# Kernel tuning notes

Measured on AMD Instinct MI355X. Metric: run time of the kernel, lower is better.

The kernel has to match this reference:

```python
import jax, jax.numpy as jnp
import numpy as np

ALPHA = 0.1        # dt / tau = 1 / 10
SIGMA_REC = 0.03
SIGMA_INP = 0.03


def setup_inputs() -> dict:
    key = jax.random.key(0)
    ks = jax.random.split(key, 7)
    n, N, num_inputs, num_outputs, T, B = 128, 1024, 6, 2, 512, 256
    u = jax.random.normal(ks[0], (num_inputs, T, B), dtype=jnp.float32)
    rec_noise = jax.random.normal(ks[1], (B, T, n), dtype=jnp.float32)
    inp_noise = jax.random.normal(ks[2], (B, T, num_inputs), dtype=jnp.float32)
    W_inp = jax.random.normal(ks[3], (n, num_inputs), dtype=jnp.float32) / np.float32(np.sqrt(num_inputs))
    # spectral-ish scaling keeps the leaky RNN stable over 512 steps
    W_rec = jax.random.normal(ks[4], (n, n), dtype=jnp.float32) * np.float32(0.9 / np.sqrt(n))
    W_out = jax.random.normal(ks[5], (num_outputs, n), dtype=jnp.float32) / np.float32(np.sqrt(n))
    # q is orthonormalized via SVD in the torch module (make_orthonormal)
    q0 = np.asarray(jax.random.uniform(ks[6], (n, N)), dtype=np.float32)
    U, _, Vh = np.linalg.svd(q0, full_matrices=False)
    q = jnp.asarray((U @ Vh).astype(np.float32))
    return dict(u=u, rec_noise=rec_noise, inp_noise=inp_noise,
                W_inp=W_inp, W_rec=W_rec, W_out=W_out, q=q)


def reference(u, rec_noise, inp_noise, W_inp, W_rec, W_out, q):
    # u: (num_inputs, T, B); noise tensors already batch-major (B, T, .)
    B = u.shape[-1]
    n = W_rec.shape[0]
    rn = jnp.sqrt(2.0 / ALPHA * SIGMA_REC ** 2) * rec_noise      # (B, T, n)
    inoise = jnp.sqrt(2.0 / ALPHA * SIGMA_INP ** 2) * inp_noise  # (B, T, num_inputs)
    ub = jnp.swapaxes(u, 0, -1)                                  # (B, T, num_inputs)
    x0 = jnp.zeros((B, n), dtype=u.dtype)                        # initial state self.x = 0

    def step(x, ins):
        u_t, in_t, rn_t = ins
        x_new = (1.0 - ALPHA) * x + ALPHA * (
            jax.nn.relu(x @ W_rec.T + (u_t + in_t) @ W_inp.T) + rn_t)
        return x_new, x_new

    # T-1 update steps using inputs at t = 0 .. T-2 (matches the torch loop)
    xs_in = (jnp.swapaxes(ub, 0, 1)[:-1],
             jnp.swapaxes(inoise, 0, 1)[:-1],
             jnp.swapaxes(rn, 0, 1)[:-1])
    _, xs = jax.lax.scan(step, x0, xs_in)                        # (T-1, B, n)
    states = jnp.concatenate([x0[:, None, :], jnp.swapaxes(xs, 0, 1)], axis=1)  # (B, T, n)

    outputs = jnp.swapaxes(states @ W_out.T, 0, -1)              # (num_outputs, T, B)
    states_embedded = jnp.swapaxes(states @ q, 0, -1)            # (N, T, B)
    return states_embedded, outputs
```

## Files before the change

kernel.cpp:

```cpp
#include <hip/hip_runtime.h>
#include <hip/hip_bf16.h>

#define T_STEPS 512
#define BATCH   256
#define NN      128
#define NEMB    1024
#define M_ROWS  (T_STEPS * BATCH)
#define NOISE_K 0.13416407864998738f
#define NB      16
#define CH      4
#define NSTEP   (T_STEPS - 1)
#define NCH     ((NSTEP + CH - 1) / CH)

typedef short s16x8 __attribute__((ext_vector_type(8)));
typedef float f32x4 __attribute__((ext_vector_type(4)));
typedef int   s32x2 __attribute__((ext_vector_type(2)));
typedef int   s32x4 __attribute__((ext_vector_type(4)));

union FragU { s32x4 i4; s16x8 s8; };

__device__ __forceinline__ unsigned short f2bf(float f) {
  union { float f; unsigned u; } v; v.f = f;
  unsigned r = v.u + 0x7fffu + ((v.u >> 16) & 1u);
  return (unsigned short)(r >> 16);
}
__device__ __forceinline__ float bf2f(unsigned short s) {
  union { unsigned u; float f; } v; v.u = ((unsigned)s) << 16;
  return v.f;
}
__device__ __forceinline__ unsigned pkbf(float lo, float hi) {
  __hip_bfloat162 h = __float22bfloat162_rn(float2{lo, hi});
  union { __hip_bfloat162 h; unsigned u; } c; c.h = h; return c.u;
}

__device__ __forceinline__ void light_barrier() {
  asm volatile("s_waitcnt lgkmcnt(0)" ::: "memory");
  __builtin_amdgcn_s_barrier();
  asm volatile("" ::: "memory");
}

__global__ __launch_bounds__(256, 1) void rnn_mfma_kernel(
    const float* __restrict__ u,
    const float* __restrict__ rec_noise,
    const float* __restrict__ inp_noise,
    const float* __restrict__ W_inp,
    const float* __restrict__ W_rec,
    unsigned short* __restrict__ states)
{
  const int b0  = blockIdx.x * NB;
  const int tid = threadIdx.x;
  const int wv  = tid >> 6;
  const int l   = tid & 63;
  const int lr  = l & 15;
  const int lg  = l >> 4;

  __shared__ char           xld[2][32 * 136];
  __shared__ float          rns[2][NB * CH * 128];
  __shared__ unsigned short uinl[NB * CH * 8];

  const int mf0 = wv * 2;
  s16x8 wA[2][5];
  #pragma unroll
  for (int mi = 0; mi < 2; ++mi) {
    const int mf = mf0 + mi;
    const float* wrow = W_rec + (size_t)(mf * 16 + lr) * NN;
    #pragma unroll
    for (int kc = 0; kc < 4; ++kc) {
      f32x4 v0 = *(const f32x4*)(wrow + kc * 32 + lg * 8);
      f32x4 v1 = *(const f32x4*)(wrow + kc * 32 + lg * 8 + 4);
      FragU f;
      f.i4 = s32x4{(int)pkbf(v0.x, v0.y), (int)pkbf(v0.z, v0.w),
                   (int)pkbf(v1.x, v1.y), (int)pkbf(v1.z, v1.w)};
      wA[mi][kc] = f.s8;
    }
    float wi[6] = {0.f, 0.f, 0.f, 0.f, 0.f, 0.f};
    if (lg == 0) {
      #pragma unroll
      for (int j = 0; j < 6; ++j) wi[j] = W_inp[(mf * 16 + lr) * 6 + j];
    }
    FragU f;
    f.i4 = s32x4{(int)pkbf(wi[0], wi[1]), (int)pkbf(wi[2], wi[3]),
                 (int)pkbf(wi[4], wi[5]), 0};
    wA[mi][4] = f.s8;
  }

  for (int i = tid; i < 1088; i += 256) ((int*)&xld[0][0])[i] = 0;
  *(s32x4*)((char*)states + (size_t)b0 * 256 + tid * 16) = s32x4{0, 0, 0, 0};

  int loff[8];
  #pragma unroll
  for (int s = 0; s < 8; ++s)
    loff[s] = (l >> 5) * 512 + (((l & 31) * 16) ^ (s << 4));

  #pragma unroll
  for (int bb = 0; bb < 4; ++bb) {
    const int b = wv * 4 + bb;
    const char* gb = (const char*)rec_noise +
                     ((size_t)(b0 + b) * T_STEPS + 0) * 512 + loff[b & 7];
    float* db = &rns[0][b * 512];
    __builtin_amdgcn_global_load_lds(
        (const __attribute__((address_space(1))) void*)gb,
        (__attribute__((address_space(3))) void*)db, 16, 0, 0);
    __builtin_amdgcn_global_load_lds(
        (const __attribute__((address_space(1))) void*)(gb + 1024),
        (__attribute__((address_space(3))) void*)(db + 256), 16, 0, 0);
  }
  float uu[6], ii[6];
  if (wv == 0) {
    #pragma unroll
    for (int j = 0; j < 6; ++j) {
      uu[j] = u[(size_t)j * (T_STEPS * BATCH) + (size_t)lg * BATCH + b0 + lr];
      ii[j] = inp_noise[((size_t)(b0 + lr) * T_STEPS + lg) * 6 + j];
    }
  }
  asm volatile("s_waitcnt vmcnt(0)" ::: "memory");
  if (wv == 0) {
    *(s32x2*)&uinl[(lr * 4 + lg) * 8] =
        s32x2{(int)pkbf(uu[0] + NOISE_K * ii[0], uu[1] + NOISE_K * ii[1]),
              (int)pkbf(uu[2] + NOISE_K * ii[2], uu[3] + NOISE_K * ii[3])};
    *(s32x2*)&uinl[(lr * 4 + lg) * 8 + 4] =
        s32x2{(int)pkbf(uu[4] + NOISE_K * ii[4], uu[5] + NOISE_K * ii[5]), 0};
  }
  __syncthreads();

  float xo[2][4];
  #pragma unroll
  for (int mi = 0; mi < 2; ++mi)
    #pragma unroll
    for (int r = 0; r < 4; ++r) xo[mi][r] = 0.f;

  for (int c = 0; c < NCH; ++c) {
    const int  cb   = c & 1;
    const bool more = (c + 1 < NCH);

    if (more) {
      const int t0n = (c + 1) * CH;
      #pragma unroll
      for (int bb = 0; bb < 4; ++bb) {
        const int b = wv * 4 + bb;
        const char* gb = (const char*)rec_noise +
                         ((size_t)(b0 + b) * T_STEPS + t0n) * 512 + loff[b & 7];
        float* db = &rns[cb ^ 1][b * 512];
        __builtin_amdgcn_global_load_lds(
            (const __attribute__((address_space(1))) void*)gb,
            (__attribute__((address_space(3))) void*)db, 16, 0, 0);
        __builtin_amdgcn_global_load_lds(
            (const __attribute__((address_space(1))) void*)(gb + 1024),
            (__attribute__((address_space(3))) void*)(db + 256), 16, 0, 0);
      }
      if (wv == 0) {
        const int tb = t0n + lg;
        #pragma unroll
        for (int j = 0; j < 6; ++j) {
          uu[j] = u[(size_t)j * (T_STEPS * BATCH) + (size_t)tb * BATCH + b0 + lr];
          ii[j] = inp_noise[((size_t)(b0 + lr) * T_STEPS + tb) * 6 + j];
        }
      }
    }

    #pragma unroll
    for (int ts = 0; ts < CH; ++ts) {
      const int t = c * CH + ts;
      if (t >= NSTEP) break;
      const int cur = t & 1, nxt = cur ^ 1;

      s16x8 xb[4];
      #pragma unroll
      for (int kc = 0; kc < 4; ++kc) {
        const char* p = xld[cur] + (kc * 8 + lg * 2) * 136 + lr * 8;
        s32x2 r1 = *(const s32x2*)p;
        s32x2 r2 = *(const s32x2*)(p + 136);
        FragU f; f.i4 = s32x4{r1.x, r1.y, r2.x, r2.y};
        xb[kc] = f.s8;
      }
      FragU uf; uf.i4 = *(const s32x4*)&uinl[(lr * 4 + ts) * 8];
      const s16x8 ub = (lg == 0) ? uf.s8 : s16x8{0, 0, 0, 0, 0, 0, 0, 0};

      unsigned short* srow =
          states + ((size_t)(t + 1) * BATCH + b0 + lr) * NN + lg * 4;

      #pragma unroll
      for (int mi = 0; mi < 2; ++mi) {
        const int mf = mf0 + mi;
        f32x4 a = f32x4{0.f, 0.f, 0.f, 0.f};
        a = __builtin_amdgcn_mfma_f32_16x16x32_bf16(wA[mi][0], xb[0], a, 0, 0, 0);
        a = __builtin_amdgcn_mfma_f32_16x16x32_bf16(wA[mi][1], xb[1], a, 0, 0, 0);
        a = __builtin_amdgcn_mfma_f32_16x16x32_bf16(wA[mi][2], xb[2], a, 0, 0, 0);
        a = __builtin_amdgcn_mfma_f32_16x16x32_bf16(wA[mi][3], xb[3], a, 0, 0, 0);
        a = __builtin_amdgcn_mfma_f32_16x16x32_bf16(wA[mi][4], ub,    a, 0, 0, 0);
        const f32x4 rn4 = *(const f32x4*)&rns[cb][lr * 512 + ts * 128 +
                               ((mf * 16 + lg * 4) ^ ((lr & 7) << 2))];
        float xn[4];
        #pragma unroll
        for (int r = 0; r < 4; ++r) {
          const float rl = fmaxf(a[r], 0.f);
          xn[r] = 0.9f * xo[mi][r] + 0.1f * (rl + NOISE_K * rn4[r]);
          xo[mi][r] = xn[r];
        }
        const s32x2 pw{(int)pkbf(xn[0], xn[1]), (int)pkbf(xn[2], xn[3])};
        *(s32x2*)(xld[nxt] + (mf * 4 + lg) * 136 + lr * 8) = pw;
        *(s32x2*)(srow + mf * 16) = pw;
      }
      light_barrier();
    }

    if (more) {
      asm volatile("s_waitcnt vmcnt(8)" ::: "memory");
      if (wv == 0) {
        *(s32x2*)&uinl[(lr * 4 + lg) * 8] =
            s32x2{(int)pkbf(uu[0] + NOISE_K * ii[0], uu[1] + NOISE_K * ii[1]),
                  (int)pkbf(uu[2] + NOISE_K * ii[2], uu[3] + NOISE_K * ii[3])};
        *(s32x2*)&uinl[(lr * 4 + lg) * 8 + 4] =
            s32x2{(int)pkbf(uu[4] + NOISE_K * ii[4], uu[5] + NOISE_K * ii[5]), 0};
      }
      light_barrier();
    }
  }
}

__global__ __launch_bounds__(256) void emb_kernel(
    const unsigned short* __restrict__ states,
    const float* __restrict__ q,
    const float* __restrict__ W_out,
    float* __restrict__ out)
{
  const int jt  = blockIdx.x;
  const int mt  = blockIdx.y;
  const int tid = threadIdx.x;
  const int w   = tid >> 6;
  const int l   = tid & 63;
  const int lg  = l >> 4;
  const int lr  = l & 15;

  __shared__ unsigned short qt[64 * 128];
  __shared__ float wos[2 * NN];

  {
    const int j  = tid & 63;
    const int k0 = tid >> 6;
    #pragma unroll
    for (int kk = k0; kk < 128; kk += 4) {
      float v = q[kk * NEMB + jt * 64 + j];
      int k8 = kk >> 3, e = kk & 7;
      qt[j * 128 + ((k8 ^ (j & 7)) << 3) + e] = f2bf(v);
    }
  }
  if (jt == 0) wos[tid] = W_out[tid];

  s16x8 afrag[2][4];
  #pragma unroll
  for (int mf = 0; mf < 2; ++mf) {
    const int m = mt * 128 + w * 32 + mf * 16 + lr;
    const unsigned short* arow = states + m * NN;
    #pragma unroll
    for (int kc = 0; kc < 4; ++kc)
      afrag[mf][kc] = *(const s16x8*)(arow + kc * 32 + lg * 8);
  }
  __syncthreads();

  f32x4 acc[2][4] = {};
  #pragma unroll
  for (int kc = 0; kc < 4; ++kc) {
    s16x8 bfrag[4];
    #pragma unroll
    for (int jf = 0; jf < 4; ++jf) {
      const int jl = jf * 16 + lr;
      bfrag[jf] = *(const s16x8*)(qt + jl * 128 + ((((kc << 2) + lg) ^ (jl & 7)) << 3));
    }
    #pragma unroll
    for (int mf = 0; mf < 2; ++mf)
      #pragma unroll
      for (int jf = 0; jf < 4; ++jf)
        acc[mf][jf] = __builtin_amdgcn_mfma_f32_16x16x32_bf16(
            afrag[mf][kc], bfrag[jf], acc[mf][jf], 0, 0, 0);
  }

  if (jt == 0) {
    #pragma unroll
    for (int mf = 0; mf < 2; ++mf) {
      float s0 = 0.f, s1 = 0.f;
      #pragma unroll
      for (int kc = 0; kc < 4; ++kc) {
        const int kb = kc * 32 + lg * 8;
        const s16x8 af = afrag[mf][kc];
        #pragma unroll
        for (int e = 0; e < 8; ++e) {
          const float x = bf2f((unsigned short)af[e]);
          s0 = fmaf(x, wos[kb + e], s0);
          s1 = fmaf(x, wos[NN + kb + e], s1);
        }
      }
      s0 += __shfl_xor(s0, 16); s0 += __shfl_xor(s0, 32);
      s1 += __shfl_xor(s1, 16); s1 += __shfl_xor(s1, 32);
      if (lg == 0) {
        const long m = (long)mt * 128 + w * 32 + mf * 16 + lr;
        out[(long)1024 * M_ROWS + m] = s0;
        out[(long)1025 * M_ROWS + m] = s1;
      }
    }
  }

  #pragma unroll
  for (int mf = 0; mf < 2; ++mf) {
    const int m = mt * 128 + w * 32 + mf * 16 + lg * 4;
    #pragma unroll
    for (int jf = 0; jf < 4; ++jf) {
      const long j = jt * 64 + jf * 16 + lr;
      *(f32x4*)&out[j * M_ROWS + m] = acc[mf][jf];
    }
  }
}

extern "C" void kernel_launch(void* const* d_in, const int* in_sizes, int n_in,
                              void* d_out, int out_size, void* d_ws, size_t ws_size,
                              hipStream_t stream) {
  const float* u         = (const float*)d_in[0];
  const float* rec_noise = (const float*)d_in[1];
  const float* inp_noise = (const float*)d_in[2];
  const float* W_inp     = (const float*)d_in[3];
  const float* W_rec     = (const float*)d_in[4];
  const float* W_out     = (const float*)d_in[5];
  const float* q         = (const float*)d_in[6];
  float* out = (float*)d_out;
  unsigned short* states = (unsigned short*)d_ws;

  rnn_mfma_kernel<<<dim3(BATCH / NB), dim3(256), 0, stream>>>(
      u, rec_noise, inp_noise, W_inp, W_rec, states);

  dim3 g2(NEMB / 64, M_ROWS / 128);
  emb_kernel<<<g2, dim3(256), 0, stream>>>(states, q, W_out, out);
}
```

Measured before the change: 501.9 us.

## Fuse recurrence and embedding GEMM into one producer-consumer persistent kernel

Result: slower. 518.3 us (+3.3%).

```diff
diff --git a/kernel.cpp b/kernel.cpp
--- a/kernel.cpp
+++ b/kernel.cpp
@@ -11,6 +11,8 @@
 #define CH      4
 #define NSTEP   (T_STEPS - 1)
 #define NCH     ((NSTEP + CH - 1) / CH)
+#define NPROD   16
+#define NCONS   240
 
 typedef short s16x8 __attribute__((ext_vector_type(8)));
 typedef float f32x4 __attribute__((ext_vector_type(4)));
@@ -39,274 +41,325 @@
   asm volatile("" ::: "memory");
 }
 
-__global__ __launch_bounds__(256, 1) void rnn_mfma_kernel(
+__device__ __forceinline__ void gstore_b64_sys(void* p, s32x2 d) {
+  asm volatile("global_store_dwordx2 %0, %1, off sc0 sc1"
+               :: "v"((unsigned long long)(__SIZE_TYPE__)p), "v"(d) : "memory");
+}
+
+struct ProdSh {
+  char           xld[2][32 * 136];
+  float          rns[2][NB * CH * 128];
+  unsigned short uinl[NB * CH * 8];
+};
+struct ConsSh {
+  unsigned short qt[64 * 128];
+  float          wos[2 * NN];
+};
+union ShU { ProdSh p; ConsSh c; };
+
+__global__ void init_prog(int* prog) {
+  if (threadIdx.x < NPROD) prog[threadIdx.x] = -1;
+}
+
+__global__ __launch_bounds__(256, 1) void fused_kernel(
     const float* __restrict__ u,
     const float* __restrict__ rec_noise,
     const float* __restrict__ inp_noise,
     const float* __restrict__ W_inp,
     const float* __restrict__ W_rec,
-    unsigned short* __restrict__ states)
-{
-  const int b0  = blockIdx.x * NB;
-  const int tid = threadIdx.x;
-  const int wv  = tid >> 6;
-  const int l   = tid & 63;
-  const int lr  = l & 15;
-  const int lg  = l >> 4;
-
-  __shared__ char           xld[2][32 * 136];
-  __shared__ float          rns[2][NB * CH * 128];
-  __shared__ unsigned short uinl[NB * CH * 8];
-
-  const int mf0 = wv * 2;
-  s16x8 wA[2][5];
-  #pragma unroll
-  for (int mi = 0; mi < 2; ++mi) {
-    const int mf = mf0 + mi;
-    const float* wrow = W_rec + (size_t)(mf * 16 + lr) * NN;
-    #pragma unroll
-    for (int kc = 0; kc < 4; ++kc) {
-      f32x4 v0 = *(const f32x4*)(wrow + kc * 32 + lg * 8);
-      f32x4 v1 = *(const f32x4*)(wrow + kc * 32 + lg * 8 + 4);
-      FragU f;
-      f.i4 = s32x4{(int)pkbf(v0.x, v0.y), (int)pkbf(v0.z, v0.w),
-                   (int)pkbf(v1.x, v1.y), (int)pkbf(v1.z, v1.w)};
-      wA[mi][kc] = f.s8;
-    }
-    float wi[6] = {0.f, 0.f, 0.f, 0.f, 0.f, 0.f};
-    if (lg == 0) {
-      #pragma unroll
-      for (int j = 0; j < 6; ++j) wi[j] = W_inp[(mf * 16 + lr) * 6 + j];
-    }
-    FragU f;
-    f.i4 = s32x4{(int)pkbf(wi[0], wi[1]), (int)pkbf(wi[2], wi[3]),
-                 (int)pkbf(wi[4], wi[5]), 0};
-    wA[mi][4] = f.s8;
-  }
-
-  for (int i = tid; i < 1088; i += 256) ((int*)&xld[0][0])[i] = 0;
-  *(s32x4*)((char*)states + (size_t)b0 * 256 + tid * 16) = s32x4{0, 0, 0, 0};
-
-  int loff[8];
-  #pragma unroll
-  for (int s = 0; s < 8; ++s)
-    loff[s] = (l >> 5) * 512 + (((l & 31) * 16) ^ (s << 4));
-
-  #pragma unroll
-  for (int bb = 0; bb < 4; ++bb) {
-    const int b = wv * 4 + bb;
-    const char* gb = (const char*)rec_noise +
-                     ((size_t)(b0 + b) * T_STEPS + 0) * 512 + loff[b & 7];
-    float* db = &rns[0][b * 512];
-    __builtin_amdgcn_global_load_lds(
-        (const __attribute__((address_space(1))) void*)gb,
-        (__attribute__((address_space(3))) void*)db, 16, 0, 0);
-    __builtin_amdgcn_global_load_lds(
-        (const __attribute__((address_space(1))) void*)(gb + 1024),
-        (__attribute__((address_space(3))) void*)(db + 256), 16, 0, 0);
-  }
-  float uu[6], ii[6];
-  if (wv == 0) {
-    #pragma unroll
-    for (int j = 0; j < 6; ++j) {
-      uu[j] = u[(size_t)j * (T_STEPS * BATCH) + (size_t)lg * BATCH + b0 + lr];
-      ii[j] = inp_noise[((size_t)(b0 + lr) * T_STEPS + lg) * 6 + j];
-    }
-  }
-  asm volatile("s_waitcnt vmcnt(0)" ::: "memory");
-  if (wv == 0) {
-    *(s32x2*)&uinl[(lr * 4 + lg) * 8] =
-        s32x2{(int)pkbf(uu[0] + NOISE_K * ii[0], uu[1] + NOISE_K * ii[1]),
-              (int)pkbf(uu[2] + NOISE_K * ii[2], uu[3] + NOISE_K * ii[3])};
-    *(s32x2*)&uinl[(lr * 4 + lg) * 8 + 4] =
-        s32x2{(int)pkbf(uu[4] + NOISE_K * ii[4], uu[5] + NOISE_K * ii[5]), 0};
-  }
-  __syncthreads();
-
-  float xo[2][4];
-  #pragma unroll
-  for (int mi = 0; mi < 2; ++mi)
-    #pragma unroll
-    for (int r = 0; r < 4; ++r) xo[mi][r] = 0.f;
-
-  for (int c = 0; c < NCH; ++c) {
-    const int  cb   = c & 1;
-    const bool more = (c + 1 < NCH);
-
-    if (more) {
-      const int t0n = (c + 1) * CH;
-      #pragma unroll
-      for (int bb = 0; bb < 4; ++bb) {
-        const int b = wv * 4 + bb;
-        const char* gb = (const char*)rec_noise +
-                         ((size_t)(b0 + b) * T_STEPS + t0n) * 512 + loff[b & 7];
-        float* db = &rns[cb ^ 1][b * 512];
-        __builtin_amdgcn_global_load_lds(
-            (const __attribute__((address_space(1))) void*)gb,
-            (__attribute__((address_space(3))) void*)db, 16, 0, 0);
-        __builtin_amdgcn_global_load_lds(
-            (const __attribute__((address_space(1))) void*)(gb + 1024),
-            (__attribute__((address_space(3))) void*)(db + 256), 16, 0, 0);
-      }
-      if (wv == 0) {
-        const int tb = t0n + lg;
-        #pragma unroll
-        for (int j = 0; j < 6; ++j) {
-          uu[j] = u[(size_t)j * (T_STEPS * BATCH) + (size_t)tb * BATCH + b0 + lr];
-          ii[j] = inp_noise[((size_t)(b0 + lr) * T_STEPS + tb) * 6 + j];
-        }
-      }
-    }
-
-    #pragma unroll
-    for (int ts = 0; ts < CH; ++ts) {
-      const int t = c * CH + ts;
-      if (t >= NSTEP) break;
-      const int cur = t & 1, nxt = cur ^ 1;
-
-      s16x8 xb[4];
-      #pragma unroll
-      for (int kc = 0; kc < 4; ++kc) {
-        const char* p = xld[cur] + (kc * 8 + lg * 2) * 136 + lr * 8;
-        s32x2 r1 = *(const s32x2*)p;
-        s32x2 r2 = *(const s32x2*)(p + 136);
-        FragU f; f.i4 = s32x4{r1.x, r1.y, r2.x, r2.y};
-        xb[kc] = f.s8;
-      }
-      FragU uf; uf.i4 = *(const s32x4*)&uinl[(lr * 4 + ts) * 8];
-      const s16x8 ub = (lg == 0) ? uf.s8 : s16x8{0, 0, 0, 0, 0, 0, 0, 0};
-
-      unsigned short* srow =
-          states + ((size_t)(t + 1) * BATCH + b0 + lr) * NN + lg * 4;
-
-      #pragma unroll
-      for (int mi = 0; mi < 2; ++mi) {
-        const int mf = mf0 + mi;
-        f32x4 a = f32x4{0.f, 0.f, 0.f, 0.f};
-        a = __builtin_amdgcn_mfma_f32_16x16x32_bf16(wA[mi][0], xb[0], a, 0, 0, 0);
-        a = __builtin_amdgcn_mfma_f32_16x16x32_bf16(wA[mi][1], xb[1], a, 0, 0, 0);
-        a = __builtin_amdgcn_mfma_f32_16x16x32_bf16(wA[mi][2], xb[2], a, 0, 0, 0);
-        a = __builtin_amdgcn_mfma_f32_16x16x32_bf16(wA[mi][3], xb[3], a, 0, 0, 0);
-        a = __builtin_amdgcn_mfma_f32_16x16x32_bf16(wA[mi][4], ub,    a, 0, 0, 0);
-        const f32x4 rn4 = *(const f32x4*)&rns[cb][lr * 512 + ts * 128 +
-                               ((mf * 16 + lg * 4) ^ ((lr & 7) << 2))];
-        float xn[4];
-        #pragma unroll
-        for (int r = 0; r < 4; ++r) {
-          const float rl = fmaxf(a[r], 0.f);
-          xn[r] = 0.9f * xo[mi][r] + 0.1f * (rl + NOISE_K * rn4[r]);
-          xo[mi][r] = xn[r];
-        }
-        const s32x2 pw{(int)pkbf(xn[0], xn[1]), (int)pkbf(xn[2], xn[3])};
-        *(s32x2*)(xld[nxt] + (mf * 4 + lg) * 136 + lr * 8) = pw;
-        *(s32x2*)(srow + mf * 16) = pw;
-      }
-      light_barrier();
-    }
-
-    if (more) {
-      asm volatile("s_waitcnt vmcnt(8)" ::: "memory");
-      if (wv == 0) {
-        *(s32x2*)&uinl[(lr * 4 + lg) * 8] =
-            s32x2{(int)pkbf(uu[0] + NOISE_K * ii[0], uu[1] + NOISE_K * ii[1]),
-                  (int)pkbf(uu[2] + NOISE_K * ii[2], uu[3] + NOISE_K * ii[3])};
-        *(s32x2*)&uinl[(lr * 4 + lg) * 8 + 4] =
-            s32x2{(int)pkbf(uu[4] + NOISE_K * ii[4], uu[5] + NOISE_K * ii[5]), 0};
-      }
-      light_barrier();
-    }
-  }
-}
-
-__global__ __launch_bounds__(256) void emb_kernel(
-    const unsigned short* __restrict__ states,
+    const float* __restrict__ W_out,
     const float* __restrict__ q,
-    const float* __restrict__ W_out,
+    unsigned short* __restrict__ states,
+    int* __restrict__ prog,
     float* __restrict__ out)
 {
-  const int jt  = blockIdx.x;
-  const int mt  = blockIdx.y;
+  __shared__ ShU sh;
+  const int bid = blockIdx.x;
   const int tid = threadIdx.x;
-  const int w   = tid >> 6;
-  const int l   = tid & 63;
-  const int lg  = l >> 4;
-  const int lr  = l & 15;
-
-  __shared__ unsigned short qt[64 * 128];
-  __shared__ float wos[2 * NN];
-
-  {
-    const int j  = tid & 63;
-    const int k0 = tid >> 6;
+
+  if (bid < NPROD) {
+    const int b0 = bid * NB;
+    const int wv = tid >> 6;
+    const int l  = tid & 63;
+    const int lr = l & 15;
+    const int lg = l >> 4;
+
+    const int mf0 = wv * 2;
+    s16x8 wA[2][5];
     #pragma unroll
-    for (int kk = k0; kk < 128; kk += 4) {
-      float v = q[kk * NEMB + jt * 64 + j];
-      int k8 = kk >> 3, e = kk & 7;
-      qt[j * 128 + ((k8 ^ (j & 7)) << 3) + e] = f2bf(v);
-    }
-  }
-  if (jt == 0) wos[tid] = W_out[tid];
-
-  s16x8 afrag[2][4];
-  #pragma unroll
-  for (int mf = 0; mf < 2; ++mf) {
-    const int m = mt * 128 + w * 32 + mf * 16 + lr;
-    const unsigned short* arow = states + m * NN;
+    for (int mi = 0; mi < 2; ++mi) {
+      const int mf = mf0 + mi;
+      const float* wrow = W_rec + (size_t)(mf * 16 + lr) * NN;
+      #pragma unroll
+      for (int kc = 0; kc < 4; ++kc) {
+        f32x4 v0 = *(const f32x4*)(wrow + kc * 32 + lg * 8);
+        f32x4 v1 = *(const f32x4*)(wrow + kc * 32 + lg * 8 + 4);
+        FragU f;
+        f.i4 = s32x4{(int)pkbf(v0.x, v0.y), (int)pkbf(v0.z, v0.w),
+                     (int)pkbf(v1.x, v1.y), (int)pkbf(v1.z, v1.w)};
+        wA[mi][kc] = f.s8;
+      }
+      float wi[6] = {0.f, 0.f, 0.f, 0.f, 0.f, 0.f};
+      if (lg == 0) {
+        #pragma unroll
+        for (int j = 0; j < 6; ++j) wi[j] = W_inp[(mf * 16 + lr) * 6 + j];
+      }
+      FragU f;
+      f.i4 = s32x4{(int)pkbf(wi[0], wi[1]), (int)pkbf(wi[2], wi[3]),
+                   (int)pkbf(wi[4], wi[5]), 0};
+      wA[mi][4] = f.s8;
+    }
+
+    for (int i = tid; i < 1088; i += 256) ((int*)&sh.p.xld[0][0])[i] = 0;
+
+    int loff[8];
     #pragma unroll
-    for (int kc = 0; kc < 4; ++kc)
-      afrag[mf][kc] = *(const s16x8*)(arow + kc * 32 + lg * 8);
-  }
-  __syncthreads();
-
-  f32x4 acc[2][4] = {};
-  #pragma unroll
-  for (int kc = 0; kc < 4; ++kc) {
-    s16x8 bfrag[4];
+    for (int s = 0; s < 8; ++s)
+      loff[s] = (l >> 5) * 512 + (((l & 31) * 16) ^ (s << 4));
+
     #pragma unroll
-    for (int jf = 0; jf < 4; ++jf) {
-      const int jl = jf * 16 + lr;
-      bfrag[jf] = *(const s16x8*)(qt + jl * 128 + ((((kc << 2) + lg) ^ (jl & 7)) << 3));
-    }
+    for (int bb = 0; bb < 4; ++bb) {
+      const int b = wv * 4 + bb;
+      const char* gb = (const char*)rec_noise +
+                       ((size_t)(b0 + b) * T_STEPS + 0) * 512 + loff[b & 7];
+      float* db = &sh.p.rns[0][b * 512];
+      __builtin_amdgcn_global_load_lds(
+          (const __attribute__((address_space(1))) void*)gb,
+          (__attribute__((address_space(3))) void*)db, 16, 0, 0);
+      __builtin_amdgcn_global_load_lds(
+          (const __attribute__((address_space(1))) void*)(gb + 1024),
+          (__attribute__((address_space(3))) void*)(db + 256), 16, 0, 0);
+    }
+    float uu[6], ii[6];
+    if (wv == 0) {
+      #pragma unroll
+      for (int j = 0; j < 6; ++j) {
+        uu[j] = u[(size_t)j * (T_STEPS * BATCH) + (size_t)lg * BATCH + b0 + lr];
+        ii[j] = inp_noise[((size_t)(b0 + lr) * T_STEPS + lg) * 6 + j];
+      }
+    }
+    asm volatile("s_waitcnt vmcnt(0)" ::: "memory");
+    if (wv == 0) {
+      *(s32x2*)&sh.p.uinl[(lr * 4 + lg) * 8] =
+          s32x2{(int)pkbf(uu[0] + NOISE_K * ii[0], uu[1] + NOISE_K * ii[1]),
+                (int)pkbf(uu[2] + NOISE_K * ii[2], uu[3] + NOISE_K * ii[3])};
+      *(s32x2*)&sh.p.uinl[(lr * 4 + lg) * 8 + 4] =
+          s32x2{(int)pkbf(uu[4] + NOISE_K * ii[4], uu[5] + NOISE_K * ii[5]), 0};
+    }
+    __syncthreads();
+
+    float xo[2][4];
     #pragma unroll
-    for (int mf = 0; mf < 2; ++mf)
-      #pragma unroll
-      for (int jf = 0; jf < 4; ++jf)
-        acc[mf][jf] = __builtin_amdgcn_mfma_f32_16x16x32_bf16(
-            afrag[mf][kc], bfrag[jf], acc[mf][jf], 0, 0, 0);
-  }
-
-  if (jt == 0) {
-    #pragma unroll
-    for (int mf = 0; mf < 2; ++mf) {
-      float s0 = 0.f, s1 = 0.f;
+    for (int mi = 0; mi < 2; ++mi)
+      #pragma unroll
+      for (int r = 0; r < 4; ++r) xo[mi][r] = 0.f;
+
+    for (int c = 0; c < NCH; ++c) {
+      const int  cb   = c & 1;
+      const bool more = (c + 1 < NCH);
+
+      if (more) {
+        const int t0n = (c + 1) * CH;
+        #pragma unroll
+        for (int bb = 0; bb < 4; ++bb) {
+          const int b = wv * 4 + bb;
+          const char* gb = (const char*)rec_noise +
+                           ((size_t)(b0 + b) * T_STEPS + t0n) * 512 + loff[b & 7];
+          float* db = &sh.p.rns[cb ^ 1][b * 512];
+          __builtin_amdgcn_global_load_lds(
+              (const __attribute__((address_space(1))) void*)gb,
+              (__attribute__((address_space(3))) void*)db, 16, 0, 0);
+          __builtin_amdgcn_global_load_lds(
+              (const __attribute__((address_space(1))) void*)(gb + 1024),
+              (__attribute__((address_space(3))) void*)(db + 256), 16, 0, 0);
+        }
+        if (wv == 0) {
+          const int tb = t0n + lg;
+          #pragma unroll
+          for (int j = 0; j < 6; ++j) {
+            uu[j] = u[(size_t)j * (T_STEPS * BATCH) + (size_t)tb * BATCH + b0 + lr];
+            ii[j] = inp_noise[((size_t)(b0 + lr) * T_STEPS + tb) * 6 + j];
+          }
+        }
+      }
+
+      #pragma unroll
+      for (int ts = 0; ts < CH; ++ts) {
+        const int t = c * CH + ts;
+        if (t >= NSTEP) break;
+        const int cur = t & 1, nxt = cur ^ 1;
+
+        s16x8 xb[4];
+        #pragma unroll
+        for (int kc = 0; kc < 4; ++kc) {
+          const char* p = sh.p.xld[cur] + (kc * 8 + lg * 2) * 136 + lr * 8;
+          s32x2 r1 = *(const s32x2*)p;
+          s32x2 r2 = *(const s32x2*)(p + 136);
+          FragU f; f.i4 = s32x4{r1.x, r1.y, r2.x, r2.y};
+          xb[kc] = f.s8;
+        }
+        FragU uf; uf.i4 = *(const s32x4*)&sh.p.uinl[(lr * 4 + ts) * 8];
+        const s16x8 ub = (lg == 0) ? uf.s8 : s16x8{0, 0, 0, 0, 0, 0, 0, 0};
+
+        unsigned short* srow =
+            states + ((size_t)(t + 1) * BATCH + b0 + lr) * NN + lg * 4;
+
+        #pragma unroll
+        for (int mi = 0; mi < 2; ++mi) {
+          const int mf = mf0 + mi;
+          f32x4 aA = f32x4{0.f, 0.f, 0.f, 0.f};
+          f32x4 aB = f32x4{0.f, 0.f, 0.f, 0.f};
+          aA = __builtin_amdgcn_mfma_f32_16x16x32_bf16(wA[mi][0], xb[0], aA, 0, 0, 0);
+          aB = __builtin_amdgcn_mfma_f32_16x16x32_bf16(wA[mi][1], xb[1], aB, 0, 0, 0);
+          aA = __builtin_amdgcn_mfma_f32_16x16x32_bf16(wA[mi][2], xb[2], aA, 0, 0, 0);
+          aB = __builtin_amdgcn_mfma_f32_16x16x32_bf16(wA[mi][3], xb[3], aB, 0, 0, 0);
+          aA = __builtin_amdgcn_mfma_f32_16x16x32_bf16(wA[mi][4], ub,    aA, 0, 0, 0);
+          const f32x4 rn4 = *(const f32x4*)&sh.p.rns[cb][lr * 512 + ts * 128 +
+                                 ((mf * 16 + lg * 4) ^ ((lr & 7) << 2))];
+          float xn[4];
+          #pragma unroll
+          for (int r = 0; r < 4; ++r) {
+            const float rl = fmaxf(aA[r] + aB[r], 0.f);
+            xn[r] = 0.9f * xo[mi][r] + 0.1f * (rl + NOISE_K * rn4[r]);
+            xo[mi][r] = xn[r];
+          }
+          const s32x2 pw{(int)pkbf(xn[0], xn[1]), (int)pkbf(xn[2], xn[3])};
+          *(s32x2*)(sh.p.xld[nxt] + (mf * 4 + lg) * 136 + lr * 8) = pw;
+          gstore_b64_sys(srow + mf * 16, pw);
+        }
+        light_barrier();
+      }
+
+      if (more) {
+        asm volatile("s_waitcnt vmcnt(8)" ::: "memory");
+        if (wv == 0) {
+          *(s32x2*)&sh.p.uinl[(lr * 4 + lg) * 8] =
+              s32x2{(int)pkbf(uu[0] + NOISE_K * ii[0], uu[1] + NOISE_K * ii[1]),
+                    (int)pkbf(uu[2] + NOISE_K * ii[2], uu[3] + NOISE_K * ii[3])};
+          *(s32x2*)&sh.p.uinl[(lr * 4 + lg) * 8 + 4] =
+              s32x2{(int)pkbf(uu[4] + NOISE_K * ii[4], uu[5] + NOISE_K * ii[5]), 0};
+        }
+        light_barrier();
+        if (tid == 0)
+          __hip_atomic_store(&prog[bid], c * CH, __ATOMIC_RELAXED,
+                             __HIP_MEMORY_SCOPE_AGENT);
+      }
+    }
+
+    asm volatile("s_waitcnt vmcnt(0)" ::: "memory");
+    light_barrier();
+    if (tid == 0)
+      __hip_atomic_store(&prog[bid], NSTEP, __ATOMIC_RELAXED,
+                         __HIP_MEMORY_SCOPE_AGENT);
+
+  } else {
+    const int k  = bid - NPROD;
+    const int jt = k & 15;
+    const int q0 = k >> 4;
+    const int w  = tid >> 6;
+    const int l  = tid & 63;
+    const int lg = l >> 4;
+    const int lr = l & 15;
+
+    {
+      const int j  = tid & 63;
+      const int k0 = tid >> 6;
+      #pragma unroll
+      for (int kk = k0; kk < 128; kk += 4) {
+        float v = q[kk * NEMB + jt * 64 + j];
+        int k8 = kk >> 3, e = kk & 7;
+        sh.c.qt[j * 128 + ((k8 ^ (j & 7)) << 3) + e] = f2bf(v);
+      }
+    }
+    if (jt == 0) sh.c.wos[tid] = W_out[tid];
+    __syncthreads();
+
+    for (int mt = q0; mt < M_ROWS / 128; mt += 15) {
+      const int t_need = mt >> 1;
+
+      if (mt >= 2) {
+        if (tid == 0) {
+          #pragma unroll 1
+          for (int g = 0; g < 8; ++g) {
+            const int gg = (mt & 1) * 8 + g;
+            while (__hip_atomic_load(&prog[gg], __ATOMIC_RELAXED,
+                                     __HIP_MEMORY_SCOPE_AGENT) < t_need)
+              __builtin_amdgcn_s_sleep(16);
+          }
+        }
+        __syncthreads();
+      }
+
+      s16x8 afrag[2][4];
+      if (mt >= 2) {
+        #pragma unroll
+        for (int mf = 0; mf < 2; ++mf) {
+          const int m = mt * 128 + w * 32 + mf * 16 + lr;
+          const unsigned short* arow = states + (size_t)m * NN;
+          #pragma unroll
+          for (int kc = 0; kc < 4; ++kc)
+            afrag[mf][kc] = *(const s16x8*)(arow + kc * 32 + lg * 8);
+        }
+      } else {
+        #pragma unroll
+        for (int mf = 0; mf < 2; ++mf)
+          #pragma unroll
+          for (int kc = 0; kc < 4; ++kc)
+            afrag[mf][kc] = s16x8{0, 0, 0, 0, 0, 0, 0, 0};
+      }
+
+      f32x4 acc[2][4] = {};
       #pragma unroll
       for (int kc = 0; kc < 4; ++kc) {
-        const int kb = kc * 32 + lg * 8;
-        const s16x8 af = afrag[mf][kc];
-        #pragma unroll
-        for (int e = 0; e < 8; ++e) {
-          const float x = bf2f((unsigned short)af[e]);
-          s0 = fmaf(x, wos[kb + e], s0);
-          s1 = fmaf(x, wos[NN + kb + e], s1);
-        }
-      }
-      s0 += __shfl_xor(s0, 16); s0 += __shfl_xor(s0, 32);
-      s1 += __shfl_xor(s1, 16); s1 += __shfl_xor(s1, 32);
-      if (lg == 0) {
-        const long m = (long)mt * 128 + w * 32 + mf * 16 + lr;
-        out[(long)1024 * M_ROWS + m] = s0;
-        out[(long)1025 * M_ROWS + m] = s1;
-      }
-    }
-  }
-
-  #pragma unroll
-  for (int mf = 0; mf < 2; ++mf) {
-    const int m = mt * 128 + w * 32 + mf * 16 + lg * 4;
-    #pragma unroll
-    for (int jf = 0; jf < 4; ++jf) {
-      const long j = jt * 64 + jf * 16 + lr;
-      *(f32x4*)&out[j * M_ROWS + m] = acc[mf][jf];
+        s16x8 bfrag[4];
+        #pragma unroll
+        for (int jf = 0; jf < 4; ++jf) {
+          const int jl = jf * 16 + lr;
+          bfrag[jf] = *(const s16x8*)(sh.c.qt + jl * 128 +
+                                      ((((kc << 2) + lg) ^ (jl & 7)) << 3));
+        }
+        #pragma unroll
+        for (int mf = 0; mf < 2; ++mf)
+          #pragma unroll
+          for (int jf = 0; jf < 4; ++jf)
+            acc[mf][jf] = __builtin_amdgcn_mfma_f32_16x16x32_bf16(
+                afrag[mf][kc], bfrag[jf], acc[mf][jf], 0, 0, 0);
+      }
+
+      if (jt == 0) {
+        #pragma unroll
+        for (int mf = 0; mf < 2; ++mf) {
+          float s0 = 0.f, s1 = 0.f;
+          #pragma unroll
+          for (int kc = 0; kc < 4; ++kc) {
+            const int kb = kc * 32 + lg * 8;
+            const s16x8 af = afrag[mf][kc];
+            #pragma unroll
+            for (int e = 0; e < 8; ++e) {
+              const float x = bf2f((unsigned short)af[e]);
+              s0 = fmaf(x, sh.c.wos[kb + e], s0);
+              s1 = fmaf(x, sh.c.wos[NN + kb + e], s1);
+            }
+          }
+          s0 += __shfl_xor(s0, 16); s0 += __shfl_xor(s0, 32);
+          s1 += __shfl_xor(s1, 16); s1 += __shfl_xor(s1, 32);
+          if (lg == 0) {
+            const long m = (long)mt * 128 + w * 32 + mf * 16 + lr;
+            out[(long)1024 * M_ROWS + m] = s0;
+            out[(long)1025 * M_ROWS + m] = s1;
+          }
+        }
+      }
+
+      #pragma unroll
+      for (int mf = 0; mf < 2; ++mf) {
+        const int m = mt * 128 + w * 32 + mf * 16 + lg * 4;
+        #pragma unroll
+        for (int jf = 0; jf < 4; ++jf) {
+          const long j = jt * 64 + jf * 16 + lr;
+          *(f32x4*)&out[j * M_ROWS + m] = acc[mf][jf];
+        }
+      }
     }
   }
 }
@@ -323,10 +376,9 @@
   const float* q         = (const float*)d_in[6];
   float* out = (float*)d_out;
   unsigned short* states = (unsigned short*)d_ws;
-
-  rnn_mfma_kernel<<<dim3(BATCH / NB), dim3(256), 0, stream>>>(
-      u, rec_noise, inp_noise, W_inp, W_rec, states);
-
-  dim3 g2(NEMB / 64, M_ROWS / 128);
-  emb_kernel<<<g2, dim3(256), 0, stream>>>(states, q, W_out, out);
-}
+  int* prog = (int*)d_ws;
+
+  init_prog<<<dim3(1), dim3(64), 0, stream>>>(prog);
+  fused_kernel<<<dim3(NPROD + NCONS), dim3(256), 0, stream>>>(
+      u, rec_noise, inp_noise, W_inp, W_rec, W_out, q, states, prog, out);
+}
```
